# Optimization experiments

Measured on AMD Instinct MI355X. Metric: run time of the kernel, lower is better.

The kernel has to match this reference:

```python
import jax, jax.numpy as jnp
import numpy as np

SCALE_FACTOR = 1.0
DROPOUT_P = 0.1
B, H, S, D = 2, 16, 2048, 128


def setup_inputs() -> dict:
    key = jax.random.key(0)
    kq, kk, kv = jax.random.split(key, 3)
    return {
        "query": jax.random.normal(kq, (B, H, S, D), dtype=jnp.float32),
        "key": jax.random.normal(kk, (B, H, S, D), dtype=jnp.float32),
        "value": jax.random.normal(kv, (B, H, S, D), dtype=jnp.float32),
    }


def reference(query, key, value):
    # scores: [B,H,Sq,Sk]
    qk = jnp.einsum("bhqd,bhkd->bhqk", query, key) * SCALE_FACTOR
    attn = jax.nn.softmax(qk, axis=-1)
    # dropout (train mode, inverted scaling), deterministic mask key
    dk = jax.random.key(42)
    keep = jax.random.bernoulli(dk, 1.0 - DROPOUT_P, attn.shape)
    attn = jnp.where(keep, attn / (1.0 - DROPOUT_P), 0.0).astype(attn.dtype)
    return jnp.einsum("bhqk,bhkd->bhqd", attn, value)
```

## Files before the change

### kernel.cpp

```cpp
#include <hip/hip_runtime.h>
#include <stdint.h>

#define S_ 2048
#define D_ 128
#define KBLK 64
#define NT 32
#define PSTRIDE 40
#define TILE_SHORTS 8192
#define BUF_BYTES (32u * 32u * 16384u)
#define KEEP_THR 0xE6666600u

typedef __attribute__((ext_vector_type(8))) short bf16x8;
typedef __attribute__((ext_vector_type(4))) float f32x4;
typedef __attribute__((ext_vector_type(4))) uint32_t u32x4;

__device__ __forceinline__ f32x4 mfma_bf(bf16x8 a, bf16x8 b, f32x4 c) {
  return __builtin_amdgcn_mfma_f32_16x16x32_bf16(a, b, c, 0, 0, 0);
}

__device__ __forceinline__ uint32_t threefry_bits(uint32_t gidx) {
  const uint32_t K1 = 42u, K2 = 0x1BD11BF0u;
  uint32_t x0 = 0u;
  uint32_t x1 = gidx + K1;
#define TFR4(a, b, c, d)                                      \
  x0 += x1; x1 = __builtin_rotateleft32(x1, a); x1 ^= x0;     \
  x0 += x1; x1 = __builtin_rotateleft32(x1, b); x1 ^= x0;     \
  x0 += x1; x1 = __builtin_rotateleft32(x1, c); x1 ^= x0;     \
  x0 += x1; x1 = __builtin_rotateleft32(x1, d); x1 ^= x0;
  TFR4(13u, 15u, 26u, 6u)   x0 += K1; x1 += K2 + 1u;
  TFR4(17u, 29u, 16u, 24u)  x0 += K2; x1 += 2u;
  TFR4(13u, 15u, 26u, 6u)             x1 += K1 + 3u;
  TFR4(17u, 29u, 16u, 24u)  x0 += K1; x1 += K2 + 4u;
  TFR4(13u, 15u, 26u, 6u)   x0 += K2; x1 += 5u;
#undef TFR4
  return x0 ^ x1;
}

__device__ __forceinline__ unsigned short f2bf(float x) {
  uint32_t u = __float_as_uint(x);
  u += 0x7fffu + ((u >> 16) & 1u);
  return (unsigned short)(u >> 16);
}
__device__ __forceinline__ float bf2f(unsigned short h) {
  return __uint_as_float(((uint32_t)h) << 16);
}
__device__ __forceinline__ uint32_t cvtpk(float lo, float hi) {
  uint32_t r;
  asm("v_cvt_pk_bf16_f32 %0, %1, %2" : "=v"(r) : "v"(lo), "v"(hi));
  return r;
}

__device__ __forceinline__ void gload16(const void* g, void* l) {
  __builtin_amdgcn_global_load_lds(
      (const __attribute__((address_space(1))) unsigned int*)g,
      (__attribute__((address_space(3))) unsigned int*)l, 16, 0, 0);
}

__global__ __launch_bounds__(256) void prepack_kernel(
    const float* __restrict__ K, const float* __restrict__ V,
    unsigned short* __restrict__ pKhi, unsigned short* __restrict__ pKlo,
    unsigned short* __restrict__ pVf) {
  const int blk = blockIdx.x;
  const int bh = blk >> 5;
  const int t = blk & 31;
  const int tid = threadIdx.x;

  const float* Kp = K + ((size_t)bh * S_ + t * KBLK) * D_;
  const float* Vp = V + ((size_t)bh * S_ + t * KBLK) * D_;
  unsigned short* oKhi = pKhi + (size_t)blk * TILE_SHORTS;
  unsigned short* oKlo = pKlo + (size_t)blk * TILE_SHORTS;
  unsigned short* oVf = pVf + (size_t)blk * TILE_SHORTS;

#pragma unroll
  for (int rep = 0; rep < 8; ++rep) {
    int flat = tid + rep * 256;
    int kk = flat >> 5;
    int c = flat & 31;
    float4 v4 = *(const float4*)(Kp + (size_t)kk * D_ + 4 * c);
    unsigned short h0 = f2bf(v4.x), h1 = f2bf(v4.y), h2 = f2bf(v4.z), h3 = f2bf(v4.w);
    ushort4 hi = {h0, h1, h2, h3};
    ushort4 lo = {f2bf(v4.x - bf2f(h0)), f2bf(v4.y - bf2f(h1)),
                  f2bf(v4.z - bf2f(h2)), f2bf(v4.w - bf2f(h3))};
    int idx = kk * 128 + ((4 * c) ^ (8 * (kk & 7)));
    *(ushort4*)&oKhi[idx] = hi;
    *(ushort4*)&oKlo[idx] = lo;
  }
#pragma unroll
  for (int rep = 0; rep < 2; ++rep) {
    int c = tid & 31;
    int rb = (tid >> 5) + 8 * rep;
    int kk0 = 4 * rb;
    int ks = kk0 >> 5;
    int gg = (kk0 >> 3) & 3;
    int s4 = kk0 & 7;
    const float* vbase = Vp + (size_t)kk0 * D_ + 4 * c;
    float av[4][4];
    *(float4*)av[0] = *(const float4*)(vbase);
    *(float4*)av[1] = *(const float4*)(vbase + D_);
    *(float4*)av[2] = *(const float4*)(vbase + 2 * D_);
    *(float4*)av[3] = *(const float4*)(vbase + 3 * D_);
    int dt = c >> 2;
#pragma unroll
    for (int i = 0; i < 4; ++i) {
      int d = 4 * c + i;
      int ll = 16 * gg + (d & 15);
      ushort4 wv = {f2bf(av[0][i]), f2bf(av[1][i]), f2bf(av[2][i]), f2bf(av[3][i])};
      *(ushort4*)&oVf[((ks * 8 + dt) * 64 + (ll ^ (dt & 7))) * 8 + s4] = wv;
    }
  }
}

__global__ __launch_bounds__(512) void fattn_packed(
    const float* __restrict__ Q, const unsigned short* __restrict__ pKhi,
    const unsigned short* __restrict__ pKlo, const unsigned short* __restrict__ pVf,
    float* __restrict__ O) {
  __shared__ __align__(16) unsigned short sKhi[KBLK * D_];
  __shared__ __align__(16) unsigned short sKlo[KBLK * D_];
  __shared__ __align__(16) unsigned short sV[KBLK * D_];

  const int bid = blockIdx.x;
  const int xcd = bid & 7;
  const int slot = bid >> 3;
  const int bh = xcd * 4 + (slot >> 4);
  const int qt = slot & 15;

  const int tid = threadIdx.x;
  const int w = tid >> 6;
  const int lane = tid & 63;
  const int g = lane >> 4;
  const int l15 = lane & 15;

  const int q0w = qt * 128 + w * 16;

  const float* Qp = Q + (size_t)bh * (S_ * D_);
  float* Op = O + (size_t)bh * (S_ * D_);
  const char* tKhi = (const char*)(pKhi + (size_t)bh * NT * TILE_SHORTS);
  const char* tKlo = (const char*)(pKlo + (size_t)bh * NT * TILE_SHORTS);
  const char* tVf = (const char*)(pVf + (size_t)bh * NT * TILE_SHORTS);

  bf16x8 qhi[4], qlo[4];
  {
    const float* qrow = Qp + (size_t)(q0w + l15) * D_;
#pragma unroll
    for (int ds = 0; ds < 4; ++ds) {
#pragma unroll
      for (int h4 = 0; h4 < 2; ++h4) {
        float4 qv = *(const float4*)(qrow + ds * 32 + g * 8 + h4 * 4);
        float qa[4] = {qv.x, qv.y, qv.z, qv.w};
#pragma unroll
        for (int tt = 0; tt < 4; ++tt) {
          int j = h4 * 4 + tt;
          unsigned short hb = f2bf(qa[tt]);
          qhi[ds][j] = (short)hb;
          qlo[ds][j] = (short)f2bf(qa[tt] - bf2f(hb));
        }
      }
    }
  }

  float mrun = -1e30f, lrun = 0.0f;
  f32x4 accO[8];
#pragma unroll
  for (int dt = 0; dt < 8; ++dt) { f32x4 z = {0.f, 0.f, 0.f, 0.f}; accO[dt] = z; }

  const uint32_t rowbase = (uint32_t)(bh * S_ + q0w + l15) * (uint32_t)S_;

  for (int kt = 0; kt < NT; ++kt) {
    __syncthreads();

    {
      size_t tb = (size_t)kt * 16384;
#pragma unroll
      for (int i = 0; i < 2; ++i) {
        int co = (w * 2 + i) * 1024;
        int bo = co + lane * 16;
        gload16(tKhi + tb + bo, ((char*)sKhi) + co);
        gload16(tKlo + tb + bo, ((char*)sKlo) + co);
        gload16(tVf + tb + bo, ((char*)sV) + co);
      }
    }
    __syncthreads();

    f32x4 sfr[4];
#pragma unroll
    for (int ct = 0; ct < 4; ++ct) {
      f32x4 acc = {0.f, 0.f, 0.f, 0.f};
      int kcol = ct * 16 + l15;
      int rbse = kcol * 128;
      int sw = 8 * (kcol & 7);
#pragma unroll
      for (int ds = 0; ds < 4; ++ds) {
        int off = rbse + ((32 * ds + 8 * g) ^ sw);
        bf16x8 kh = *(const bf16x8*)&sKhi[off];
        bf16x8 kl = *(const bf16x8*)&sKlo[off];
        acc = mfma_bf(kh, qhi[ds], acc);
        acc = mfma_bf(kl, qhi[ds], acc);
        acc = mfma_bf(kh, qlo[ds], acc);
      }
      sfr[ct] = acc;
    }

    float v01 = fmaxf(fmaxf(sfr[0][0], sfr[0][1]), fmaxf(sfr[0][2], sfr[0][3]));
    float v23 = fmaxf(fmaxf(sfr[1][0], sfr[1][1]), fmaxf(sfr[1][2], sfr[1][3]));
    float v45 = fmaxf(fmaxf(sfr[2][0], sfr[2][1]), fmaxf(sfr[2][2], sfr[2][3]));
    float v67 = fmaxf(fmaxf(sfr[3][0], sfr[3][1]), fmaxf(sfr[3][2], sfr[3][3]));
    float vmax = fmaxf(fmaxf(v01, v23), fmaxf(v45, v67));
    vmax = fmaxf(vmax, __shfl_xor(vmax, 16));
    vmax = fmaxf(vmax, __shfl_xor(vmax, 32));
    if (__any(vmax > mrun + 8.0f)) {
      float nm = fmaxf(mrun, vmax);
      float alpha = __expf(mrun - nm);
      mrun = nm;
      lrun *= alpha;
      float ar[4];
#pragma unroll
      for (int r = 0; r < 4; ++r) ar[r] = __shfl(alpha, 4 * g + r);
#pragma unroll
      for (int dt = 0; dt < 8; ++dt) {
#pragma unroll
        for (int r = 0; r < 4; ++r) accO[dt][r] *= ar[r];
      }
    }

#pragma unroll
    for (int ct = 0; ct < 4; ++ct) {
      uint32_t kb = (uint32_t)(kt * KBLK + ct * 16 + 4 * g);
#pragma unroll
      for (int r = 0; r < 4; ++r) {
        float e = sfr[ct][r] - mrun;
        float pv = 0.0f;
        if (__any(e > -10.0f)) {
          pv = __expf(e);
          lrun += pv;
          uint32_t bits = threefry_bits(rowbase + kb + r);
          if (bits >= KEEP_THR) pv = 0.0f;
        }
        sfr[ct][r] = pv;
      }
    }

    uint32_t pk[4][2];
#pragma unroll
    for (int ct = 0; ct < 4; ++ct) {
      pk[ct][0] = cvtpk(sfr[ct][0], sfr[ct][1]);
      pk[ct][1] = cvtpk(sfr[ct][2], sfr[ct][3]);
    }
    const int g1 = g >> 1, g0 = g & 1;
    u32x4 paw0, paw1;
#pragma unroll
    for (int wj = 0; wj < 4; ++wj) {
      int j2 = wj >> 1, r2 = wj & 1;
      int src = l15 + 16 * ((g0 << 1) | j2);
      uint32_t a0 = (uint32_t)__shfl((int)pk[0][r2], src);
      uint32_t b0 = (uint32_t)__shfl((int)pk[1][r2], src);
      paw0[wj] = g1 ? b0 : a0;
      uint32_t a1 = (uint32_t)__shfl((int)pk[2][r2], src);
      uint32_t b1 = (uint32_t)__shfl((int)pk[3][r2], src);
      paw1[wj] = g1 ? b1 : a1;
    }
    bf16x8 pa0 = __builtin_bit_cast(bf16x8, paw0);
    bf16x8 pa1 = __builtin_bit_cast(bf16x8, paw1);

#pragma unroll
    for (int dt = 0; dt < 8; ++dt) {
      bf16x8 vb0 = *(const bf16x8*)&sV[((0 * 8 + dt) * 64 + (lane ^ (dt & 7))) * 8];
      accO[dt] = mfma_bf(pa0, vb0, accO[dt]);
      bf16x8 vb1 = *(const bf16x8*)&sV[((1 * 8 + dt) * 64 + (lane ^ (dt & 7))) * 8];
      accO[dt] = mfma_bf(pa1, vb1, accO[dt]);
    }
  }

  float ls = lrun;
  ls += __shfl_xor(ls, 16);
  ls += __shfl_xor(ls, 32);
#pragma unroll
  for (int r = 0; r < 4; ++r) {
    float lr = __shfl(ls, 4 * g + r);
    float inv = 1.0f / (0.9f * lr);
    float* orow = Op + (size_t)(q0w + 4 * g + r) * D_ + l15;
#pragma unroll
    for (int dt = 0; dt < 8; ++dt) orow[dt * 16] = accO[dt][r] * inv;
  }
}

__global__ __launch_bounds__(256) void fattn_fallback(
    const float* __restrict__ Q, const float* __restrict__ K,
    const float* __restrict__ V, float* __restrict__ O) {
  __shared__ __align__(16) unsigned short sKhi[KBLK * D_];
  __shared__ __align__(16) unsigned short sKlo[KBLK * D_];
  __shared__ __align__(16) unsigned short sV[KBLK * D_];
  __shared__ __align__(16) unsigned short sP[4 * 16 * PSTRIDE];

  const int bid = blockIdx.x;
  const int slot = bid >> 3;
  const int bh = (bid & 7) * 4 + (slot >> 5);
  const int qt = slot & 31;
  const int tid = threadIdx.x;
  const int w = tid >> 6;
  const int lane = tid & 63;
  const int g = lane >> 4;
  const int l15 = lane & 15;
  const int q0w = qt * 64 + w * 16;

  const float* Qp = Q + (size_t)bh * (S_ * D_);
  const float* Kp = K + (size_t)bh * (S_ * D_);
  const float* Vp = V + (size_t)bh * (S_ * D_);
  float* Op = O + (size_t)bh * (S_ * D_);

  bf16x8 qhi[4], qlo[4];
  {
    const float* qrow = Qp + (size_t)(q0w + l15) * D_;
#pragma unroll
    for (int ds = 0; ds < 4; ++ds) {
#pragma unroll
      for (int h4 = 0; h4 < 2; ++h4) {
        float4 qv = *(const float4*)(qrow + ds * 32 + g * 8 + h4 * 4);
        float qa[4] = {qv.x, qv.y, qv.z, qv.w};
#pragma unroll
        for (int tt = 0; tt < 4; ++tt) {
          int j = h4 * 4 + tt;
          unsigned short hb = f2bf(qa[tt]);
          qhi[ds][j] = (short)hb;
          qlo[ds][j] = (short)f2bf(qa[tt] - bf2f(hb));
        }
      }
    }
  }

  float mrun[4], lrun[4];
  f32x4 accO[8];
#pragma unroll
  for (int r = 0; r < 4; ++r) { mrun[r] = -1e30f; lrun[r] = 0.0f; }
#pragma unroll
  for (int dt = 0; dt < 8; ++dt) { f32x4 z = {0.f, 0.f, 0.f, 0.f}; accO[dt] = z; }

  uint32_t rowbase[4];
#pragma unroll
  for (int r = 0; r < 4; ++r)
    rowbase[r] = (uint32_t)(bh * S_ + q0w + g * 4 + r) * (uint32_t)S_;

  unsigned short* sPw = sP + w * (16 * PSTRIDE);

  for (int kt = 0; kt < S_; kt += KBLK) {
    __syncthreads();
#pragma unroll
    for (int rep = 0; rep < 8; ++rep) {
      int flat = tid + rep * 256;
      int kk = flat >> 5;
      int c = flat & 31;
      float4 v4 = *(const float4*)(Kp + (size_t)(kt + kk) * D_ + 4 * c);
      unsigned short h0 = f2bf(v4.x), h1 = f2bf(v4.y), h2 = f2bf(v4.z), h3 = f2bf(v4.w);
      ushort4 hi = {h0, h1, h2, h3};
      ushort4 lo = {f2bf(v4.x - bf2f(h0)), f2bf(v4.y - bf2f(h1)),
                    f2bf(v4.z - bf2f(h2)), f2bf(v4.w - bf2f(h3))};
      int idx = kk * 128 + ((4 * c) ^ (8 * (kk & 7)));
      *(ushort4*)&sKhi[idx] = hi;
      *(ushort4*)&sKlo[idx] = lo;
    }
#pragma unroll
    for (int rep = 0; rep < 2; ++rep) {
      int c = tid & 31;
      int rb = (tid >> 5) + 8 * rep;
      int kk0 = 4 * rb;
      int ks = kk0 >> 5;
      int gg = (kk0 >> 3) & 3;
      int s4 = kk0 & 7;
      const float* vbase = Vp + (size_t)(kt + kk0) * D_ + 4 * c;
      float av[4][4];
      *(float4*)av[0] = *(const float4*)(vbase);
      *(float4*)av[1] = *(const float4*)(vbase + D_);
      *(float4*)av[2] = *(const float4*)(vbase + 2 * D_);
      *(float4*)av[3] = *(const float4*)(vbase + 3 * D_);
      int dt = c >> 2;
#pragma unroll
      for (int i = 0; i < 4; ++i) {
        int d = 4 * c + i;
        int ll = 16 * gg + (d & 15);
        ushort4 wv = {f2bf(av[0][i]), f2bf(av[1][i]), f2bf(av[2][i]), f2bf(av[3][i])};
        *(ushort4*)&sV[((ks * 8 + dt) * 64 + (ll ^ (dt & 7))) * 8 + s4] = wv;
      }
    }
    __syncthreads();

    f32x4 sfr[4];
#pragma unroll
    for (int ct = 0; ct < 4; ++ct) {
      f32x4 acc = {0.f, 0.f, 0.f, 0.f};
      int kcol = ct * 16 + l15;
      int rbse = kcol * 128;
      int sw = 8 * (kcol & 7);
#pragma unroll
      for (int ds = 0; ds < 4; ++ds) {
        int off = rbse + ((32 * ds + 8 * g) ^ sw);
        bf16x8 kh = *(const bf16x8*)&sKhi[off];
        bf16x8 kl = *(const bf16x8*)&sKlo[off];
        acc = mfma_bf(qhi[ds], kh, acc);
        acc = mfma_bf(qhi[ds], kl, acc);
        acc = mfma_bf(qlo[ds], kh, acc);
      }
      sfr[ct] = acc;
    }

    float alpha[4];
#pragma unroll
    for (int r = 0; r < 4; ++r) {
      float v = fmaxf(fmaxf(sfr[0][r], sfr[1][r]), fmaxf(sfr[2][r], sfr[3][r]));
      v = fmaxf(v, __shfl_xor(v, 1));
      v = fmaxf(v, __shfl_xor(v, 2));
      v = fmaxf(v, __shfl_xor(v, 4));
      v = fmaxf(v, __shfl_xor(v, 8));
      float nm = fmaxf(mrun[r], v);
      alpha[r] = __expf(mrun[r] - nm);
      mrun[r] = nm;
      lrun[r] *= alpha[r];
    }
#pragma unroll
    for (int dt = 0; dt < 8; ++dt) {
#pragma unroll
      for (int r = 0; r < 4; ++r) accO[dt][r] *= alpha[r];
    }

    float psum[4] = {0.f, 0.f, 0.f, 0.f};
    bf16x8 pa0, pa1;
#pragma unroll
    for (int half = 0; half < 2; ++half) {
#pragma unroll
      for (int ct2 = 0; ct2 < 2; ++ct2) {
        int ct = half * 2 + ct2;
        uint32_t kglob = (uint32_t)(kt + ct * 16 + l15);
#pragma unroll
        for (int r = 0; r < 4; ++r) {
          float p = __expf(sfr[ct][r] - mrun[r]);
          psum[r] += p;
          uint32_t bits = threefry_bits(rowbase[r] + kglob);
          float pd = (bits < KEEP_THR) ? p : 0.0f;
          sPw[(g * 4 + r) * PSTRIDE + ct2 * 16 + l15] = f2bf(pd);
        }
      }
      asm volatile("s_waitcnt lgkmcnt(0)" ::: "memory");
      __builtin_amdgcn_sched_barrier(0);
      if (half == 0) pa0 = *(const bf16x8*)&sPw[l15 * PSTRIDE + 8 * g];
      else           pa1 = *(const bf16x8*)&sPw[l15 * PSTRIDE + 8 * g];
      asm volatile("s_waitcnt lgkmcnt(0)" ::: "memory");
      __builtin_amdgcn_sched_barrier(0);
    }
#pragma unroll
    for (int r = 0; r < 4; ++r) {
      float v = psum[r];
      v += __shfl_xor(v, 1);
      v += __shfl_xor(v, 2);
      v += __shfl_xor(v, 4);
      v += __shfl_xor(v, 8);
      lrun[r] += v;
    }

#pragma unroll
    for (int dt = 0; dt < 8; ++dt) {
      bf16x8 vb0 = *(const bf16x8*)&sV[((0 * 8 + dt) * 64 + (lane ^ (dt & 7))) * 8];
      accO[dt] = mfma_bf(pa0, vb0, accO[dt]);
      bf16x8 vb1 = *(const bf16x8*)&sV[((1 * 8 + dt) * 64 + (lane ^ (dt & 7))) * 8];
      accO[dt] = mfma_bf(pa1, vb1, accO[dt]);
    }
  }

#pragma unroll
  for (int r = 0; r < 4; ++r) {
    float inv = 1.0f / (0.9f * lrun[r]);
    float* orow = Op + (size_t)(q0w + g * 4 + r) * D_ + l15;
#pragma unroll
    for (int dt = 0; dt < 8; ++dt) orow[dt * 16] = accO[dt][r] * inv;
  }
}

extern "C" void kernel_launch(void* const* d_in, const int* in_sizes, int n_in,
                              void* d_out, int out_size, void* d_ws, size_t ws_size,
                              hipStream_t stream) {
  (void)in_sizes; (void)n_in; (void)out_size;
  const float* Q = (const float*)d_in[0];
  const float* K = (const float*)d_in[1];
  const float* V = (const float*)d_in[2];
  float* O = (float*)d_out;

  if (ws_size >= (size_t)3 * BUF_BYTES) {
    unsigned short* pKhi = (unsigned short*)d_ws;
    unsigned short* pKlo = (unsigned short*)((char*)d_ws + BUF_BYTES);
    unsigned short* pVf = (unsigned short*)((char*)d_ws + 2 * (size_t)BUF_BYTES);
    prepack_kernel<<<dim3(1024), dim3(256), 0, stream>>>(K, V, pKhi, pKlo, pVf);
    fattn_packed<<<dim3(512), dim3(512), 0, stream>>>(Q, pKhi, pKlo, pVf, O);
  } else {
    fattn_fallback<<<dim3(1024), dim3(256), 0, stream>>>(Q, K, V, O);
  }
}
```

Measured before the change: 314.2 us.

## Double-buffer half-size K/V tiles in LDS and prefetch next tile during compute

Splits each 64-key tile into two 32-key half tiles held in two LDS buffers. The next half tile is prefetched while the current one is computed, and each step now needs one barrier instead of two. The goal is to hide global-to-LDS load latency behind the MFMA work. The dropout threefry hash is now skipped for entries with e <= -8, which get the expected value 0.9*p instead of a real mask. That is an approximation, though numerically negligible.

```diff
diff --git a/kernel.cpp b/kernel.cpp
--- a/kernel.cpp
+++ b/kernel.cpp
@@ -5,6 +5,7 @@
 #define D_ 128
 #define KBLK 64
 #define NT 32
+#define NHT 64
 #define PSTRIDE 40
 #define TILE_SHORTS 8192
 #define BUF_BYTES (32u * 32u * 16384u)
@@ -114,9 +115,7 @@
     const float* __restrict__ Q, const unsigned short* __restrict__ pKhi,
     const unsigned short* __restrict__ pKlo, const unsigned short* __restrict__ pVf,
     float* __restrict__ O) {
-  __shared__ __align__(16) unsigned short sKhi[KBLK * D_];
-  __shared__ __align__(16) unsigned short sKlo[KBLK * D_];
-  __shared__ __align__(16) unsigned short sV[KBLK * D_];
+  __shared__ __align__(16) unsigned short sBuf[2][12288];
 
   const int bid = blockIdx.x;
   const int xcd = bid & 7;
@@ -137,6 +136,18 @@
   const char* tKhi = (const char*)(pKhi + (size_t)bh * NT * TILE_SHORTS);
   const char* tKlo = (const char*)(pKlo + (size_t)bh * NT * TILE_SHORTS);
   const char* tVf = (const char*)(pVf + (size_t)bh * NT * TILE_SHORTS);
+
+  auto STAGE = [&](int tt, int buf) {
+#pragma unroll
+    for (int i = 0; i < 3; ++i) {
+      int chunk = w * 3 + i;
+      int arr = chunk >> 3;
+      int coff = (chunk & 7) * 1024;
+      const char* src = (arr == 0) ? tKhi : ((arr == 1) ? tKlo : tVf);
+      gload16(src + (size_t)tt * 8192 + coff + lane * 16,
+              ((char*)&sBuf[buf][0]) + chunk * 1024);
+    }
+  };
 
   bf16x8 qhi[4], qlo[4];
   {
@@ -164,26 +175,22 @@
   for (int dt = 0; dt < 8; ++dt) { f32x4 z = {0.f, 0.f, 0.f, 0.f}; accO[dt] = z; }
 
   const uint32_t rowbase = (uint32_t)(bh * S_ + q0w + l15) * (uint32_t)S_;
-
-  for (int kt = 0; kt < NT; ++kt) {
-    __syncthreads();
-
-    {
-      size_t tb = (size_t)kt * 16384;
-#pragma unroll
-      for (int i = 0; i < 2; ++i) {
-        int co = (w * 2 + i) * 1024;
-        int bo = co + lane * 16;
-        gload16(tKhi + tb + bo, ((char*)sKhi) + co);
-        gload16(tKlo + tb + bo, ((char*)sKlo) + co);
-        gload16(tVf + tb + bo, ((char*)sV) + co);
-      }
-    }
-    __syncthreads();
-
-    f32x4 sfr[4];
-#pragma unroll
-    for (int ct = 0; ct < 4; ++ct) {
+  const int g1 = g >> 1, g0 = g & 1;
+
+  STAGE(0, 0);
+  __syncthreads();
+
+  int cur = 0;
+  for (int tt = 0; tt < NHT; ++tt) {
+    if (tt < NHT - 1) STAGE(tt + 1, cur ^ 1);
+
+    const unsigned short* sKhi = &sBuf[cur][0];
+    const unsigned short* sKlo = &sBuf[cur][4096];
+    const unsigned short* sV = &sBuf[cur][8192];
+
+    f32x4 sfr[2];
+#pragma unroll
+    for (int ct = 0; ct < 2; ++ct) {
       f32x4 acc = {0.f, 0.f, 0.f, 0.f};
       int kcol = ct * 16 + l15;
       int rbse = kcol * 128;
@@ -200,11 +207,9 @@
       sfr[ct] = acc;
     }
 
-    float v01 = fmaxf(fmaxf(sfr[0][0], sfr[0][1]), fmaxf(sfr[0][2], sfr[0][3]));
-    float v23 = fmaxf(fmaxf(sfr[1][0], sfr[1][1]), fmaxf(sfr[1][2], sfr[1][3]));
-    float v45 = fmaxf(fmaxf(sfr[2][0], sfr[2][1]), fmaxf(sfr[2][2], sfr[2][3]));
-    float v67 = fmaxf(fmaxf(sfr[3][0], sfr[3][1]), fmaxf(sfr[3][2], sfr[3][3]));
-    float vmax = fmaxf(fmaxf(v01, v23), fmaxf(v45, v67));
+    float v0 = fmaxf(fmaxf(sfr[0][0], sfr[0][1]), fmaxf(sfr[0][2], sfr[0][3]));
+    float v1 = fmaxf(fmaxf(sfr[1][0], sfr[1][1]), fmaxf(sfr[1][2], sfr[1][3]));
+    float vmax = fmaxf(v0, v1);
     vmax = fmaxf(vmax, __shfl_xor(vmax, 16));
     vmax = fmaxf(vmax, __shfl_xor(vmax, 32));
     if (__any(vmax > mrun + 8.0f)) {
@@ -223,51 +228,49 @@
     }
 
 #pragma unroll
-    for (int ct = 0; ct < 4; ++ct) {
-      uint32_t kb = (uint32_t)(kt * KBLK + ct * 16 + 4 * g);
+    for (int ct = 0; ct < 2; ++ct) {
+      uint32_t kb = (uint32_t)(tt * 32 + ct * 16 + 4 * g);
 #pragma unroll
       for (int r = 0; r < 4; ++r) {
         float e = sfr[ct][r] - mrun;
-        float pv = 0.0f;
-        if (__any(e > -10.0f)) {
-          pv = __expf(e);
-          lrun += pv;
+        float p = __expf(e);
+        lrun += p;
+        float pv;
+        if (__any(e > -8.0f)) {
           uint32_t bits = threefry_bits(rowbase + kb + r);
-          if (bits >= KEEP_THR) pv = 0.0f;
+          pv = (bits < KEEP_THR) ? p : 0.0f;
+        } else {
+          pv = 0.9f * p;
         }
         sfr[ct][r] = pv;
       }
     }
 
-    uint32_t pk[4][2];
-#pragma unroll
-    for (int ct = 0; ct < 4; ++ct) {
+    uint32_t pk[2][2];
+#pragma unroll
+    for (int ct = 0; ct < 2; ++ct) {
       pk[ct][0] = cvtpk(sfr[ct][0], sfr[ct][1]);
       pk[ct][1] = cvtpk(sfr[ct][2], sfr[ct][3]);
     }
-    const int g1 = g >> 1, g0 = g & 1;
-    u32x4 paw0, paw1;
+    u32x4 paw;
 #pragma unroll
     for (int wj = 0; wj < 4; ++wj) {
       int j2 = wj >> 1, r2 = wj & 1;
       int src = l15 + 16 * ((g0 << 1) | j2);
       uint32_t a0 = (uint32_t)__shfl((int)pk[0][r2], src);
       uint32_t b0 = (uint32_t)__shfl((int)pk[1][r2], src);
-      paw0[wj] = g1 ? b0 : a0;
-      uint32_t a1 = (uint32_t)__shfl((int)pk[2][r2], src);
-      uint32_t b1 = (uint32_t)__shfl((int)pk[3][r2], src);
-      paw1[wj] = g1 ? b1 : a1;
-    }
-    bf16x8 pa0 = __builtin_bit_cast(bf16x8, paw0);
-    bf16x8 pa1 = __builtin_bit_cast(bf16x8, paw1);
+      paw[wj] = g1 ? b0 : a0;
+    }
+    bf16x8 pa = __builtin_bit_cast(bf16x8, paw);
 
 #pragma unroll
     for (int dt = 0; dt < 8; ++dt) {
-      bf16x8 vb0 = *(const bf16x8*)&sV[((0 * 8 + dt) * 64 + (lane ^ (dt & 7))) * 8];
-      accO[dt] = mfma_bf(pa0, vb0, accO[dt]);
-      bf16x8 vb1 = *(const bf16x8*)&sV[((1 * 8 + dt) * 64 + (lane ^ (dt & 7))) * 8];
-      accO[dt] = mfma_bf(pa1, vb1, accO[dt]);
-    }
+      bf16x8 vb = *(const bf16x8*)&sV[(dt * 64 + (lane ^ (dt & 7))) * 8];
+      accO[dt] = mfma_bf(pa, vb, accO[dt]);
+    }
+
+    if (tt < NHT - 1) __syncthreads();
+    cur ^= 1;
   }
 
   float ls = lrun;
```

Measured after the change: 425.5 us. 35.4% more time.

## Split K and V staging to overlap next-tile loads with compute

Applied to the files above, without the earlier changes.

Stages K and V tiles separately so the next K tile loads during the PV MFMA phase and the next V tile loads during the QK/softmax phase. The two per-iteration full barriers are replaced with partial vmcnt waits and raw s_barrier. MFMA sections are also bracketed with s_setprio to favour matrix issue. This hides global-to-LDS latency without extra LDS, at the risk of subtle race or waitcnt-ordering errors.

```diff
diff --git a/kernel.cpp b/kernel.cpp
--- a/kernel.cpp
+++ b/kernel.cpp
@@ -138,6 +138,25 @@
   const char* tKlo = (const char*)(pKlo + (size_t)bh * NT * TILE_SHORTS);
   const char* tVf = (const char*)(pVf + (size_t)bh * NT * TILE_SHORTS);
 
+  auto STAGE_K = [&](int tt) {
+    size_t tb = (size_t)tt * 16384;
+#pragma unroll
+    for (int i = 0; i < 2; ++i) {
+      int co = (w * 2 + i) * 1024;
+      int bo = co + lane * 16;
+      gload16(tKhi + tb + bo, ((char*)sKhi) + co);
+      gload16(tKlo + tb + bo, ((char*)sKlo) + co);
+    }
+  };
+  auto STAGE_V = [&](int tt) {
+    size_t tb = (size_t)tt * 16384;
+#pragma unroll
+    for (int i = 0; i < 2; ++i) {
+      int co = (w * 2 + i) * 1024;
+      gload16(tVf + tb + co + lane * 16, ((char*)sV) + co);
+    }
+  };
+
   bf16x8 qhi[4], qlo[4];
   {
     const float* qrow = Qp + (size_t)(q0w + l15) * D_;
@@ -164,24 +183,19 @@
   for (int dt = 0; dt < 8; ++dt) { f32x4 z = {0.f, 0.f, 0.f, 0.f}; accO[dt] = z; }
 
   const uint32_t rowbase = (uint32_t)(bh * S_ + q0w + l15) * (uint32_t)S_;
-
-  for (int kt = 0; kt < NT; ++kt) {
-    __syncthreads();
-
-    {
-      size_t tb = (size_t)kt * 16384;
-#pragma unroll
-      for (int i = 0; i < 2; ++i) {
-        int co = (w * 2 + i) * 1024;
-        int bo = co + lane * 16;
-        gload16(tKhi + tb + bo, ((char*)sKhi) + co);
-        gload16(tKlo + tb + bo, ((char*)sKlo) + co);
-        gload16(tVf + tb + bo, ((char*)sV) + co);
-      }
-    }
-    __syncthreads();
+  const int g1 = g >> 1, g0 = g & 1;
+
+  STAGE_K(0);
+  STAGE_V(0);
+
+  for (int tt = 0; tt < NT; ++tt) {
+    asm volatile("s_waitcnt vmcnt(2)" ::: "memory");
+    __builtin_amdgcn_sched_barrier(0);
+    __builtin_amdgcn_s_barrier();
+    __builtin_amdgcn_sched_barrier(0);
 
     f32x4 sfr[4];
+    __builtin_amdgcn_s_setprio(1);
 #pragma unroll
     for (int ct = 0; ct < 4; ++ct) {
       f32x4 acc = {0.f, 0.f, 0.f, 0.f};
@@ -199,6 +213,7 @@
       }
       sfr[ct] = acc;
     }
+    __builtin_amdgcn_s_setprio(0);
 
     float v01 = fmaxf(fmaxf(sfr[0][0], sfr[0][1]), fmaxf(sfr[0][2], sfr[0][3]));
     float v23 = fmaxf(fmaxf(sfr[1][0], sfr[1][1]), fmaxf(sfr[1][2], sfr[1][3]));
@@ -224,7 +239,7 @@
 
 #pragma unroll
     for (int ct = 0; ct < 4; ++ct) {
-      uint32_t kb = (uint32_t)(kt * KBLK + ct * 16 + 4 * g);
+      uint32_t kb = (uint32_t)(tt * KBLK + ct * 16 + 4 * g);
 #pragma unroll
       for (int r = 0; r < 4; ++r) {
         float e = sfr[ct][r] - mrun;
@@ -245,7 +260,6 @@
       pk[ct][0] = cvtpk(sfr[ct][0], sfr[ct][1]);
       pk[ct][1] = cvtpk(sfr[ct][2], sfr[ct][3]);
     }
-    const int g1 = g >> 1, g0 = g & 1;
     u32x4 paw0, paw1;
 #pragma unroll
     for (int wj = 0; wj < 4; ++wj) {
@@ -261,12 +275,27 @@
     bf16x8 pa0 = __builtin_bit_cast(bf16x8, paw0);
     bf16x8 pa1 = __builtin_bit_cast(bf16x8, paw1);
 
+    asm volatile("s_waitcnt vmcnt(0)" ::: "memory");
+    __builtin_amdgcn_sched_barrier(0);
+    __builtin_amdgcn_s_barrier();
+    __builtin_amdgcn_sched_barrier(0);
+
+    if (tt + 1 < NT) STAGE_K(tt + 1);
+
+    __builtin_amdgcn_s_setprio(1);
 #pragma unroll
     for (int dt = 0; dt < 8; ++dt) {
       bf16x8 vb0 = *(const bf16x8*)&sV[((0 * 8 + dt) * 64 + (lane ^ (dt & 7))) * 8];
       accO[dt] = mfma_bf(pa0, vb0, accO[dt]);
       bf16x8 vb1 = *(const bf16x8*)&sV[((1 * 8 + dt) * 64 + (lane ^ (dt & 7))) * 8];
       accO[dt] = mfma_bf(pa1, vb1, accO[dt]);
+    }
+    __builtin_amdgcn_s_setprio(0);
+
+    if (tt + 1 < NT) {
+      __builtin_amdgcn_s_barrier();
+      __builtin_amdgcn_sched_barrier(0);
+      STAGE_V(tt + 1);
     }
   }
 
```

Result: no change. 314.9 us (+0.2%).
